# Optimization experiments

Hardware: AMD Instinct MI355X
Metric: run time of the kernel (lower is better)

Reference implementation:

```python
import jax, jax.numpy as jnp
import numpy as np

NUM_EMBEDDINGS = 512
EMBEDDING_DIM = 64


def setup_inputs() -> dict:
    key = jax.random.key(0)
    k1, k2 = jax.random.split(key)
    z = jax.random.normal(k1, (32, EMBEDDING_DIM, 64, 64), dtype=jnp.float32)
    lim = 1.0 / NUM_EMBEDDINGS
    emb = jax.random.uniform(k2, (NUM_EMBEDDINGS, EMBEDDING_DIM),
                             minval=-lim, maxval=lim, dtype=jnp.float32)
    return {"z": z, "emb": emb}


def reference(z, emb):
    # z: [B, C, H, W] with C == embedding_dim
    B, C, H, W = z.shape
    z_hwc = jnp.transpose(z, (0, 2, 3, 1))            # [B, H, W, C]
    flat = z_hwc.reshape(-1, C)                       # [N, C]
    dists = (jnp.sum(flat * flat, axis=1, keepdims=True)
             + jnp.sum(emb * emb, axis=1)
             - 2.0 * flat @ emb.T)                    # [N, K]
    idx = jnp.argmin(dists, axis=1)                   # [N]
    quantized = emb[idx].reshape(z_hwc.shape)         # gather == one-hot matmul
    quantized_st = z_hwc + jax.lax.stop_gradient(quantized - z_hwc)
    q_chw = jnp.transpose(quantized, (0, 3, 1, 2))    # [B, C, H, W]
    qst_chw = jnp.transpose(quantized_st, (0, 3, 1, 2))
    vq_loss = jnp.mean((jax.lax.stop_gradient(q_chw) - z) ** 2)
    commitment_loss = jnp.mean((q_chw - jax.lax.stop_gradient(z)) ** 2)
    return (qst_chw, vq_loss, commitment_loss, idx.reshape(B, H, W))
```

## Files before the change

kernel.cpp:

```cpp
#include <hip/hip_runtime.h>
#include <math.h>

#define NUM_EMB 512
#define EDIM 64
#define BATCH 32
#define HW 4096
#define NROWS (BATCH * HW)
#define NQ (NROWS * EDIM)

#define XOFF 0
#define EOFF 16384
#define T2OFF 32768
#define T1OFF 33280
#define CBOFF 16384
#define CKOFF (16384 + 4096)
#define SFLOATS 33536

__device__ __forceinline__ float pairwise8_64(const float* v) {
    float r0 = v[0], r1 = v[1], r2 = v[2], r3 = v[3];
    float r4 = v[4], r5 = v[5], r6 = v[6], r7 = v[7];
#pragma unroll
    for (int i = 8; i < 64; i += 8) {
        r0 = __fadd_rn(r0, v[i + 0]);
        r1 = __fadd_rn(r1, v[i + 1]);
        r2 = __fadd_rn(r2, v[i + 2]);
        r3 = __fadd_rn(r3, v[i + 3]);
        r4 = __fadd_rn(r4, v[i + 4]);
        r5 = __fadd_rn(r5, v[i + 5]);
        r6 = __fadd_rn(r6, v[i + 6]);
        r7 = __fadd_rn(r7, v[i + 7]);
    }
    return __fadd_rn(__fadd_rn(__fadd_rn(r0, r1), __fadd_rn(r2, r3)),
                     __fadd_rn(__fadd_rn(r4, r5), __fadd_rn(r6, r7)));
}

__global__ void vq_prep(const float* __restrict__ emb, float* __restrict__ ws_f) {
    int k = blockIdx.x * blockDim.x + threadIdx.x;
    if (k == 0) ws_f[0] = 0.0f;
    if (k < NUM_EMB) {
        const float* e = emb + k * EDIM;
        float sq[EDIM];
#pragma unroll
        for (int c = 0; c < EDIM; ++c) sq[c] = __fmul_rn(e[c], e[c]);
        ws_f[8 + k] = pairwise8_64(sq);
    }
}

__global__ __launch_bounds__(512, 2) void vq_main(const float* __restrict__ z,
                                                  const float* __restrict__ emb,
                                                  float* __restrict__ out,
                                                  float* __restrict__ ws_f) {
    __shared__ float S[SFLOATS];
    const int tid = threadIdx.x;
    const int rt  = tid & 31;
    const int kt  = tid >> 5;
    const int row0 = rt * 4;
    const int bb  = blockIdx.x;
    const int b   = bb >> 4;
    const int hwb = (bb & 15) << 8;

    const float* zb = z + (size_t)b * (EDIM * HW) + hwb;

    {
        const int r = tid & 255, ch = tid >> 8;
#pragma unroll
        for (int j = 0; j < 32; ++j) {
            const int c = ch * 32 + j;
            S[XOFF + c * 256 + r] = zb[(size_t)c * HW + r];
        }
    }
    S[T2OFF + tid] = ws_f[8 + tid];
    __syncthreads();

    if (tid < 256) {
        const float* xr = &S[XOFF + tid];
        float q0 = __fmul_rn(xr[0 * 256], xr[0 * 256]);
        float q1 = __fmul_rn(xr[1 * 256], xr[1 * 256]);
        float q2 = __fmul_rn(xr[2 * 256], xr[2 * 256]);
        float q3 = __fmul_rn(xr[3 * 256], xr[3 * 256]);
        float q4 = __fmul_rn(xr[4 * 256], xr[4 * 256]);
        float q5 = __fmul_rn(xr[5 * 256], xr[5 * 256]);
        float q6 = __fmul_rn(xr[6 * 256], xr[6 * 256]);
        float q7 = __fmul_rn(xr[7 * 256], xr[7 * 256]);
#pragma unroll
        for (int m = 1; m < 8; ++m) {
            float v0 = xr[(8 * m + 0) * 256], v1 = xr[(8 * m + 1) * 256];
            float v2 = xr[(8 * m + 2) * 256], v3 = xr[(8 * m + 3) * 256];
            float v4 = xr[(8 * m + 4) * 256], v5 = xr[(8 * m + 5) * 256];
            float v6 = xr[(8 * m + 6) * 256], v7 = xr[(8 * m + 7) * 256];
            q0 = __fadd_rn(q0, __fmul_rn(v0, v0));
            q1 = __fadd_rn(q1, __fmul_rn(v1, v1));
            q2 = __fadd_rn(q2, __fmul_rn(v2, v2));
            q3 = __fadd_rn(q3, __fmul_rn(v3, v3));
            q4 = __fadd_rn(q4, __fmul_rn(v4, v4));
            q5 = __fadd_rn(q5, __fmul_rn(v5, v5));
            q6 = __fadd_rn(q6, __fmul_rn(v6, v6));
            q7 = __fadd_rn(q7, __fmul_rn(v7, v7));
        }
        S[T1OFF + tid] = __fadd_rn(__fadd_rn(__fadd_rn(q0, q1), __fadd_rn(q2, q3)),
                                   __fadd_rn(__fadd_rn(q4, q5), __fadd_rn(q6, q7)));
    }
    __syncthreads();

    float t1r[8];
#pragma unroll
    for (int i = 0; i < 4; ++i) t1r[i] = S[T1OFF + row0 + i];
#pragma unroll
    for (int i = 4; i < 8; ++i) t1r[i] = S[T1OFF + 128 + row0 + (i - 4)];

    float best[8];
    int   bki[8];
#pragma unroll
    for (int i = 0; i < 8; ++i) { best[i] = INFINITY; bki[i] = 0; }

    for (int p = 0; p < 2; ++p) {
        {
            const int k = tid & 255, ch = tid >> 8;
            const float4* er = (const float4*)(emb + (size_t)(p * 256 + k) * EDIM);
#pragma unroll
            for (int j = 0; j < 8; ++j) {
                const float4 v = er[ch * 8 + j];
                const int c = ch * 32 + j * 4;
                S[EOFF + (c + 0) * 256 + k] = v.x;
                S[EOFF + (c + 1) * 256 + k] = v.y;
                S[EOFF + (c + 2) * 256 + k] = v.z;
                S[EOFF + (c + 3) * 256 + k] = v.w;
            }
        }
        __syncthreads();

#pragma unroll
        for (int blk = 0; blk < 2; ++blk) {
            const int kb = kt * 16 + blk * 8;
            float acc[8][8];
#pragma unroll
            for (int i = 0; i < 8; ++i)
#pragma unroll
                for (int j = 0; j < 8; ++j) acc[i][j] = 0.0f;

#pragma unroll 4
            for (int c = 0; c < 64; ++c) {
                const float4 xa = *(const float4*)&S[XOFF + c * 256 + row0];
                const float4 xb = *(const float4*)&S[XOFF + c * 256 + 128 + row0];
                const float4 ea = *(const float4*)&S[EOFF + c * 256 + kb];
                const float4 eb = *(const float4*)&S[EOFF + c * 256 + kb + 4];
#define ROW(i, xv) \
                acc[i][0] = __fmaf_rn(xv, ea.x, acc[i][0]); \
                acc[i][1] = __fmaf_rn(xv, ea.y, acc[i][1]); \
                acc[i][2] = __fmaf_rn(xv, ea.z, acc[i][2]); \
                acc[i][3] = __fmaf_rn(xv, ea.w, acc[i][3]); \
                acc[i][4] = __fmaf_rn(xv, eb.x, acc[i][4]); \
                acc[i][5] = __fmaf_rn(xv, eb.y, acc[i][5]); \
                acc[i][6] = __fmaf_rn(xv, eb.z, acc[i][6]); \
                acc[i][7] = __fmaf_rn(xv, eb.w, acc[i][7]);
                ROW(0, xa.x) ROW(1, xa.y) ROW(2, xa.z) ROW(3, xa.w)
                ROW(4, xb.x) ROW(5, xb.y) ROW(6, xb.z) ROW(7, xb.w)
#undef ROW
            }

#pragma unroll
            for (int j = 0; j < 8; ++j) {
                const int kg = p * 256 + kb + j;
                const float t2k = S[T2OFF + kg];
#pragma unroll
                for (int i = 0; i < 8; ++i) {
                    float d = __fsub_rn(__fadd_rn(t1r[i], t2k),
                                        __fmul_rn(2.0f, acc[i][j]));
                    if (d < best[i]) { best[i] = d; bki[i] = kg; }
                }
            }
        }
        __syncthreads();
    }

#pragma unroll
    for (int i = 0; i < 4; ++i) {
        S[CBOFF + kt * 256 + row0 + i] = best[i];
        ((int*)S)[CKOFF + kt * 256 + row0 + i] = bki[i];
    }
#pragma unroll
    for (int i = 4; i < 8; ++i) {
        S[CBOFF + kt * 256 + 128 + row0 + (i - 4)] = best[i];
        ((int*)S)[CKOFF + kt * 256 + 128 + row0 + (i - 4)] = bki[i];
    }
    __syncthreads();

    if (tid < 256) {
        const int row = tid;
        float B = INFINITY;
        int   K = 0;
#pragma unroll
        for (int q = 0; q < 16; ++q) {
            const float bq = S[CBOFF + q * 256 + row];
            const int   kq = ((int*)S)[CKOFF + q * 256 + row];
            if (bq < B || (bq == B && kq < K)) { B = bq; K = kq; }
        }

        const float* eb = emb + (size_t)K * EDIM;
        const float* xc = &S[XOFF + row];
        float s = 0.0f;
#pragma unroll
        for (int c = 0; c < 64; ++c) {
            const float x = xc[c * 256];
            const float f = __fsub_rn(eb[c], x);
            out[((size_t)b * EDIM + c) * HW + hwb + row] = __fadd_rn(x, f);
            s = __fmaf_rn(f, f, s);
        }
        out[(size_t)NQ + 2 + bb * 256 + row] = (float)K;

#pragma unroll
        for (int off = 32; off > 0; off >>= 1) s += __shfl_down(s, off);
        if ((tid & 63) == 0) atomicAdd(ws_f, s);
    }
}

__global__ void vq_final(const float* __restrict__ ws_f, float* __restrict__ out) {
    float m = ws_f[0] * (1.0f / (float)NQ);
    out[NQ + 0] = m;
    out[NQ + 1] = m;
}

extern "C" void kernel_launch(void* const* d_in, const int* in_sizes, int n_in,
                              void* d_out, int out_size, void* d_ws, size_t ws_size,
                              hipStream_t stream) {
    const float* z = (const float*)d_in[0];
    const float* emb = (const float*)d_in[1];
    float* out = (float*)d_out;
    float* ws_f = (float*)d_ws;

    hipLaunchKernelGGL(vq_prep, dim3(1), dim3(512), 0, stream, emb, ws_f);
    hipLaunchKernelGGL(vq_main, dim3(NROWS / 256), dim3(512), 0, stream, z, emb, out, ws_f);
    hipLaunchKernelGGL(vq_final, dim3(1), dim3(1), 0, stream, ws_f, out);
}
```

Measured before the change: 152.2 us.

## Read codebook directly from global memory, drop LDS staging, raise occupancy

Codebook vectors are no longer staged into shared memory. Each thread now loads its 8 codewords straight from global memory (cache-served, wave-uniform per 32-thread group) as float4s. This removes the per-pass codebook transpose and its barriers, halves the LDS footprint, and raises the launch bound to 4 blocks per CU. The candidate-reduction buffers now reuse the x region, so the epilogue rereads z from global memory. The costs are more global/cache traffic in the inner loop, register pressure under the tighter launch bound, and an extra read of z.

```diff
diff --git a/kernel.cpp b/kernel.cpp
--- a/kernel.cpp
+++ b/kernel.cpp
@@ -9,12 +9,11 @@
 #define NQ (NROWS * EDIM)
 
 #define XOFF 0
-#define EOFF 16384
-#define T2OFF 32768
-#define T1OFF 33280
-#define CBOFF 16384
-#define CKOFF (16384 + 4096)
-#define SFLOATS 33536
+#define T2OFF 16384
+#define T1OFF 16896
+#define CBOFF 0
+#define CKOFF 4096
+#define SFLOATS 17152
 
 __device__ __forceinline__ float pairwise8_64(const float* v) {
     float r0 = v[0], r1 = v[1], r2 = v[2], r3 = v[3];
@@ -46,7 +45,7 @@
     }
 }
 
-__global__ __launch_bounds__(512, 2) void vq_main(const float* __restrict__ z,
+__global__ __launch_bounds__(512, 4) void vq_main(const float* __restrict__ z,
                                                   const float* __restrict__ emb,
                                                   float* __restrict__ out,
                                                   float* __restrict__ ws_f) {
@@ -113,65 +112,69 @@
 #pragma unroll
     for (int i = 0; i < 8; ++i) { best[i] = INFINITY; bki[i] = 0; }
 
-    for (int p = 0; p < 2; ++p) {
-        {
-            const int k = tid & 255, ch = tid >> 8;
-            const float4* er = (const float4*)(emb + (size_t)(p * 256 + k) * EDIM);
-#pragma unroll
-            for (int j = 0; j < 8; ++j) {
-                const float4 v = er[ch * 8 + j];
-                const int c = ch * 32 + j * 4;
-                S[EOFF + (c + 0) * 256 + k] = v.x;
-                S[EOFF + (c + 1) * 256 + k] = v.y;
-                S[EOFF + (c + 2) * 256 + k] = v.z;
-                S[EOFF + (c + 3) * 256 + k] = v.w;
-            }
-        }
-        __syncthreads();
-
-#pragma unroll
-        for (int blk = 0; blk < 2; ++blk) {
-            const int kb = kt * 16 + blk * 8;
-            float acc[8][8];
-#pragma unroll
-            for (int i = 0; i < 8; ++i)
-#pragma unroll
-                for (int j = 0; j < 8; ++j) acc[i][j] = 0.0f;
+#pragma unroll 1
+    for (int s = 0; s < 4; ++s) {
+        const int k0 = kt * 32 + s * 8;
+        const float4* __restrict__ eb4 = (const float4*)(emb + (size_t)k0 * EDIM);
+
+        float acc[8][8];
+#pragma unroll
+        for (int i = 0; i < 8; ++i)
+#pragma unroll
+            for (int j = 0; j < 8; ++j) acc[i][j] = 0.0f;
 
 #pragma unroll 4
-            for (int c = 0; c < 64; ++c) {
+        for (int cc = 0; cc < 16; ++cc) {
+            float4 e0 = eb4[0 * 16 + cc];
+            float4 e1 = eb4[1 * 16 + cc];
+            float4 e2 = eb4[2 * 16 + cc];
+            float4 e3 = eb4[3 * 16 + cc];
+            float4 e4 = eb4[4 * 16 + cc];
+            float4 e5 = eb4[5 * 16 + cc];
+            float4 e6 = eb4[6 * 16 + cc];
+            float4 e7 = eb4[7 * 16 + cc];
+#pragma unroll
+            for (int q = 0; q < 4; ++q) {
+                const int c = cc * 4 + q;
                 const float4 xa = *(const float4*)&S[XOFF + c * 256 + row0];
                 const float4 xb = *(const float4*)&S[XOFF + c * 256 + 128 + row0];
-                const float4 ea = *(const float4*)&S[EOFF + c * 256 + kb];
-                const float4 eb = *(const float4*)&S[EOFF + c * 256 + kb + 4];
+                const float eq0 = (q == 0) ? e0.x : (q == 1) ? e0.y : (q == 2) ? e0.z : e0.w;
+                const float eq1 = (q == 0) ? e1.x : (q == 1) ? e1.y : (q == 2) ? e1.z : e1.w;
+                const float eq2 = (q == 0) ? e2.x : (q == 1) ? e2.y : (q == 2) ? e2.z : e2.w;
+                const float eq3 = (q == 0) ? e3.x : (q == 1) ? e3.y : (q == 2) ? e3.z : e3.w;
+                const float eq4 = (q == 0) ? e4.x : (q == 1) ? e4.y : (q == 2) ? e4.z : e4.w;
+                const float eq5 = (q == 0) ? e5.x : (q == 1) ? e5.y : (q == 2) ? e5.z : e5.w;
+                const float eq6 = (q == 0) ? e6.x : (q == 1) ? e6.y : (q == 2) ? e6.z : e6.w;
+                const float eq7 = (q == 0) ? e7.x : (q == 1) ? e7.y : (q == 2) ? e7.z : e7.w;
 #define ROW(i, xv) \
-                acc[i][0] = __fmaf_rn(xv, ea.x, acc[i][0]); \
-                acc[i][1] = __fmaf_rn(xv, ea.y, acc[i][1]); \
-                acc[i][2] = __fmaf_rn(xv, ea.z, acc[i][2]); \
-                acc[i][3] = __fmaf_rn(xv, ea.w, acc[i][3]); \
-                acc[i][4] = __fmaf_rn(xv, eb.x, acc[i][4]); \
-                acc[i][5] = __fmaf_rn(xv, eb.y, acc[i][5]); \
-                acc[i][6] = __fmaf_rn(xv, eb.z, acc[i][6]); \
-                acc[i][7] = __fmaf_rn(xv, eb.w, acc[i][7]);
+                acc[i][0] = __fmaf_rn(xv, eq0, acc[i][0]); \
+                acc[i][1] = __fmaf_rn(xv, eq1, acc[i][1]); \
+                acc[i][2] = __fmaf_rn(xv, eq2, acc[i][2]); \
+                acc[i][3] = __fmaf_rn(xv, eq3, acc[i][3]); \
+                acc[i][4] = __fmaf_rn(xv, eq4, acc[i][4]); \
+                acc[i][5] = __fmaf_rn(xv, eq5, acc[i][5]); \
+                acc[i][6] = __fmaf_rn(xv, eq6, acc[i][6]); \
+                acc[i][7] = __fmaf_rn(xv, eq7, acc[i][7]);
                 ROW(0, xa.x) ROW(1, xa.y) ROW(2, xa.z) ROW(3, xa.w)
                 ROW(4, xb.x) ROW(5, xb.y) ROW(6, xb.z) ROW(7, xb.w)
 #undef ROW
             }
-
-#pragma unroll
-            for (int j = 0; j < 8; ++j) {
-                const int kg = p * 256 + kb + j;
-                const float t2k = S[T2OFF + kg];
-#pragma unroll
-                for (int i = 0; i < 8; ++i) {
-                    float d = __fsub_rn(__fadd_rn(t1r[i], t2k),
-                                        __fmul_rn(2.0f, acc[i][j]));
-                    if (d < best[i]) { best[i] = d; bki[i] = kg; }
-                }
+        }
+
+#pragma unroll
+        for (int j = 0; j < 8; ++j) {
+            const int kg = k0 + j;
+            const float t2k = S[T2OFF + kg];
+#pragma unroll
+            for (int i = 0; i < 8; ++i) {
+                float d = __fsub_rn(__fadd_rn(t1r[i], t2k),
+                                    __fmul_rn(2.0f, acc[i][j]));
+                if (d < best[i]) { best[i] = d; bki[i] = kg; }
             }
         }
-        __syncthreads();
-    }
+    }
+
+    __syncthreads();
 
 #pragma unroll
     for (int i = 0; i < 4; ++i) {
@@ -197,11 +200,10 @@
         }
 
         const float* eb = emb + (size_t)K * EDIM;
-        const float* xc = &S[XOFF + row];
         float s = 0.0f;
 #pragma unroll
         for (int c = 0; c < 64; ++c) {
-            const float x = xc[c * 256];
+            const float x = zb[(size_t)c * HW + row];
             const float f = __fsub_rn(eb[c], x);
             out[((size_t)b * EDIM + c) * HW + hwb + row] = __fadd_rn(x, f);
             s = __fmaf_rn(f, f, s);
```

Result: slower. 323.5 us (+112.6%).

## Software-pipeline LDS reads in distance GEMM with inline asm double buffering

Applied to the files above, without the earlier changes.

Replaces the compiler-scheduled inner c-loop of the distance computation with a fully unrolled, hand-pipelined sequence. Inline ds_read_b128 instructions with immediate offsets load the next channel's operands into a second register set while FMAs run on the current set, and explicit lgkmcnt waits plus sched_barrier stop the compiler from reordering. The intent is to hide LDS latency behind the FMA work. In exchange it raises register pressure (two operand buffers), grows the code size, and disables unrolling of the outer p/blk loops.

```diff
diff --git a/kernel.cpp b/kernel.cpp
--- a/kernel.cpp
+++ b/kernel.cpp
@@ -15,6 +15,8 @@
 #define CBOFF 16384
 #define CKOFF (16384 + 4096)
 #define SFLOATS 33536
+
+typedef float f32x4 __attribute__((ext_vector_type(4)));
 
 __device__ __forceinline__ float pairwise8_64(const float* v) {
     float r0 = v[0], r1 = v[1], r2 = v[2], r3 = v[3];
@@ -45,6 +47,40 @@
         ws_f[8 + k] = pairwise8_64(sq);
     }
 }
+
+#define READ(P, C) \
+    asm volatile("ds_read_b128 %0, %1 offset:%2" \
+                 : "=v"(P##xa) : "v"(bx), "n"((C) * 1024)); \
+    asm volatile("ds_read_b128 %0, %1 offset:%2" \
+                 : "=v"(P##xb) : "v"(bx), "n"((C) * 1024 + 512)); \
+    asm volatile("ds_read_b128 %0, %1 offset:%2" \
+                 : "=v"(P##ea) : "v"(be), "n"((C) * 1024)); \
+    asm volatile("ds_read_b128 %0, %1 offset:%2" \
+                 : "=v"(P##eb) : "v"(be), "n"((C) * 1024 + 16));
+
+#define WAIT4 asm volatile("s_waitcnt lgkmcnt(4)"); __builtin_amdgcn_sched_barrier(0);
+#define WAIT0 asm volatile("s_waitcnt lgkmcnt(0)"); __builtin_amdgcn_sched_barrier(0);
+
+#define ROW1(i, xv, P) \
+    acc[i][0] = __fmaf_rn(xv, P##ea.x, acc[i][0]); \
+    acc[i][1] = __fmaf_rn(xv, P##ea.y, acc[i][1]); \
+    acc[i][2] = __fmaf_rn(xv, P##ea.z, acc[i][2]); \
+    acc[i][3] = __fmaf_rn(xv, P##ea.w, acc[i][3]); \
+    acc[i][4] = __fmaf_rn(xv, P##eb.x, acc[i][4]); \
+    acc[i][5] = __fmaf_rn(xv, P##eb.y, acc[i][5]); \
+    acc[i][6] = __fmaf_rn(xv, P##eb.z, acc[i][6]); \
+    acc[i][7] = __fmaf_rn(xv, P##eb.w, acc[i][7]);
+#define FMA64(P) \
+    ROW1(0, P##xa.x, P) ROW1(1, P##xa.y, P) ROW1(2, P##xa.z, P) ROW1(3, P##xa.w, P) \
+    ROW1(4, P##xb.x, P) ROW1(5, P##xb.y, P) ROW1(6, P##xb.z, P) ROW1(7, P##xb.w, P)
+
+#define ST(m) \
+    READ(B_, 2 * m + 1) WAIT4 FMA64(A_) \
+    READ(A_, 2 * m + 2) WAIT4 FMA64(B_)
+#define DO31(F) \
+  F(0) F(1) F(2) F(3) F(4) F(5) F(6) F(7) F(8) F(9) F(10) F(11) F(12) F(13) \
+  F(14) F(15) F(16) F(17) F(18) F(19) F(20) F(21) F(22) F(23) F(24) F(25) \
+  F(26) F(27) F(28) F(29) F(30)
 
 __global__ __launch_bounds__(512, 2) void vq_main(const float* __restrict__ z,
                                                   const float* __restrict__ emb,
@@ -113,13 +149,14 @@
 #pragma unroll
     for (int i = 0; i < 8; ++i) { best[i] = INFINITY; bki[i] = 0; }
 
+#pragma unroll 1
     for (int p = 0; p < 2; ++p) {
         {
             const int k = tid & 255, ch = tid >> 8;
-            const float4* er = (const float4*)(emb + (size_t)(p * 256 + k) * EDIM);
+            const f32x4* er = (const f32x4*)(emb + (size_t)(p * 256 + k) * EDIM);
 #pragma unroll
             for (int j = 0; j < 8; ++j) {
-                const float4 v = er[ch * 8 + j];
+                const f32x4 v = er[ch * 8 + j];
                 const int c = ch * 32 + j * 4;
                 S[EOFF + (c + 0) * 256 + k] = v.x;
                 S[EOFF + (c + 1) * 256 + k] = v.y;
@@ -129,34 +166,25 @@
         }
         __syncthreads();
 
-#pragma unroll
+#pragma unroll 1
         for (int blk = 0; blk < 2; ++blk) {
             const int kb = kt * 16 + blk * 8;
+            const unsigned bx = (unsigned)(uintptr_t)&S[XOFF + row0];
+            const unsigned be = (unsigned)(uintptr_t)&S[EOFF + kb];
+
             float acc[8][8];
 #pragma unroll
             for (int i = 0; i < 8; ++i)
 #pragma unroll
                 for (int j = 0; j < 8; ++j) acc[i][j] = 0.0f;
 
-#pragma unroll 4
-            for (int c = 0; c < 64; ++c) {
-                const float4 xa = *(const float4*)&S[XOFF + c * 256 + row0];
-                const float4 xb = *(const float4*)&S[XOFF + c * 256 + 128 + row0];
-                const float4 ea = *(const float4*)&S[EOFF + c * 256 + kb];
-                const float4 eb = *(const float4*)&S[EOFF + c * 256 + kb + 4];
-#define ROW(i, xv) \
-                acc[i][0] = __fmaf_rn(xv, ea.x, acc[i][0]); \
-                acc[i][1] = __fmaf_rn(xv, ea.y, acc[i][1]); \
-                acc[i][2] = __fmaf_rn(xv, ea.z, acc[i][2]); \
-                acc[i][3] = __fmaf_rn(xv, ea.w, acc[i][3]); \
-                acc[i][4] = __fmaf_rn(xv, eb.x, acc[i][4]); \
-                acc[i][5] = __fmaf_rn(xv, eb.y, acc[i][5]); \
-                acc[i][6] = __fmaf_rn(xv, eb.z, acc[i][6]); \
-                acc[i][7] = __fmaf_rn(xv, eb.w, acc[i][7]);
-                ROW(0, xa.x) ROW(1, xa.y) ROW(2, xa.z) ROW(3, xa.w)
-                ROW(4, xb.x) ROW(5, xb.y) ROW(6, xb.z) ROW(7, xb.w)
-#undef ROW
-            }
+            f32x4 A_xa, A_xb, A_ea, A_eb;
+            f32x4 B_xa, B_xb, B_ea, B_eb;
+
+            READ(A_, 0)
+            DO31(ST)
+            READ(B_, 63) WAIT4 FMA64(A_)
+            WAIT0 FMA64(B_)
 
 #pragma unroll
             for (int j = 0; j < 8; ++j) {
```

New measurement: 142.7 us, median of 2. 1.07x faster.
